# Optimization experiments

Measured on AMD Instinct MI355X. Metric: run time of the kernel, lower is better.

The kernel has to match this reference:

```python
import jax, jax.numpy as jnp
import numpy as np

B, T, C = 8, 2048, 1024
CONTEXT_SIZE = T  # repo ties context_size to sequence length of the mask


def setup_inputs() -> dict:
    key = jax.random.key(0)
    ks = jax.random.split(key, 7)
    s = 1.0 / np.sqrt(C)
    return {
        "x": jax.random.normal(ks[0], (B, T, C), dtype=jnp.float32),
        "Wq": jax.random.normal(ks[1], (C, C), dtype=jnp.float32) * s,
        "bq": jax.random.normal(ks[2], (C,), dtype=jnp.float32) * s,
        "Wk": jax.random.normal(ks[3], (C, C), dtype=jnp.float32) * s,
        "bk": jax.random.normal(ks[4], (C,), dtype=jnp.float32) * s,
        "Wv": jax.random.normal(ks[5], (C, C), dtype=jnp.float32) * s,
        "bv": jax.random.normal(ks[6], (C,), dtype=jnp.float32) * s,
    }


def reference(x, Wq, bq, Wk, bk, Wv, bv):
    # x: [B, T, C]; weights stored as [in, out] so y = x @ W + b (same math as nn.Linear)
    Tlen = x.shape[1]
    q = x @ Wq + bq
    k = x @ Wk + bk
    v = x @ Wv + bv
    # NOTE: original scales by context_size**-0.5 (seq-length based), not head-dim
    scale = jnp.asarray(CONTEXT_SIZE, x.dtype) ** -0.5
    scores = jnp.einsum("btc,bsc->bts", q, k) * scale  # [B, T, T]
    causal = jnp.tril(jnp.ones((Tlen, Tlen), dtype=bool))
    scores = jnp.where(causal, scores, -jnp.inf)
    attn = jax.nn.softmax(scores, axis=-1)
    return jnp.einsum("bts,bsc->btc", attn, v)
```

## Files before the change

### kernel.cpp

```cpp
#include <hip/hip_runtime.h>

#define B_SZ 8
#define T_SZ 2048
#define C_SZ 1024

typedef __attribute__((ext_vector_type(8))) short short8;
typedef __attribute__((ext_vector_type(8))) unsigned short ushort8;
typedef __attribute__((ext_vector_type(4))) float f32x4;

__device__ __forceinline__ unsigned short f2bf(float x) {
  union { float f; unsigned u; } v; v.f = x;
  unsigned r = v.u + 0x7FFFu + ((v.u >> 16) & 1u);
  return (unsigned short)(r >> 16);
}
__device__ __forceinline__ float bf2f(unsigned short h) {
  union { unsigned u; float f; } v; v.u = ((unsigned)h) << 16;
  return v.f;
}

__device__ __forceinline__ void gload16(const void* g, void* l) {
  __builtin_amdgcn_global_load_lds(
      (const __attribute__((address_space(1))) unsigned int*)(uintptr_t)g,
      (__attribute__((address_space(3))) unsigned int*)(uintptr_t)l, 16, 0, 0);
}

__device__ __forceinline__ int xcd_swz(int orig, int nwg) {
  return (orig & 7) * (nwg >> 3) + (orig >> 3);
}

#define WAITV(N) asm volatile("s_waitcnt vmcnt(" #N ")" ::: "memory")
#define BAR1                            \
  {                                     \
    asm volatile("" ::: "memory");      \
    __builtin_amdgcn_s_barrier();       \
    __builtin_amdgcn_sched_barrier(0);  \
    asm volatile("" ::: "memory");      \
  }
#define BAR2                            \
  {                                     \
    asm volatile("" ::: "memory");      \
    __builtin_amdgcn_s_barrier();       \
    asm volatile("" ::: "memory");      \
  }

template <int LDA, int LDB>
__device__ __forceinline__ void nt8p(const unsigned short* __restrict__ Ab,
                                     const unsigned short* __restrict__ Bb,
                                     const int NT, unsigned short* lds,
                                     f32x4 (&acc)[2][4][4]) {
  const int lane = threadIdx.x & 63;
  const int wid = threadIdx.x >> 6;
  const int wr = wid >> 2;
  const int wc = wid & 3;
  const int fr = lane & 15;
  const int fq = lane >> 4;

  const int aslot = ((lane & 7) ^ (lane >> 3)) * 8;
  const int rr0 = (wid * 2 + 0) * 8 + (lane >> 3);
  const int rr1 = (wid * 2 + 1) * 8 + (lane >> 3);
  const unsigned short* pA0 =
      Ab + (size_t)((rr0 >> 6) * 128 + (rr0 & 63)) * LDA + aslot;
  const unsigned short* pA1 =
      Ab + (size_t)((rr1 >> 6) * 128 + (rr1 & 63)) * LDA + aslot;
  const int bslot = ((lane & 3) ^ ((lane >> 3) & 3)) * 8;
  const unsigned short* pB0 =
      Bb + (size_t)((wid * 2 + 0) * 16 + (lane >> 2)) * LDB + bslot;
  const unsigned short* pB1 =
      Bb + (size_t)((wid * 2 + 1) * 16 + (lane >> 2)) * LDB + bslot;
  const int ldsC0 = (wid * 2 + 0) * 512;
  const int ldsC1 = (wid * 2 + 1) * 512;

  const int arb = wr * 4096 + fr * 64;
  const int asw0 = ((0 * 4 + fq) ^ (fr & 7)) * 8;
  const int asw1 = ((1 * 4 + fq) ^ (fr & 7)) * 8;
  const int brb =
      16384 + (wc * 64 + fr) * 32 + ((fq ^ ((fr >> 1) & 3)) * 8);

#define STG_A(d, h, kt)                                           \
  {                                                               \
    gload16(pA0 + (size_t)(h) * 64 * LDA + (size_t)(kt) * 64,     \
            lds + (d) * 32768 + (h) * 8192 + ldsC0);              \
    gload16(pA1 + (size_t)(h) * 64 * LDA + (size_t)(kt) * 64,     \
            lds + (d) * 32768 + (h) * 8192 + ldsC1);              \
  }
#define STG_B(d, kh, kt)                                          \
  {                                                               \
    gload16(pB0 + (kh) * 32 + (size_t)(kt) * 64,                  \
            lds + (d) * 32768 + 16384 + (kh) * 8192 + ldsC0);     \
    gload16(pB1 + (kh) * 32 + (size_t)(kt) * 64,                  \
            lds + (d) * 32768 + 16384 + (kh) * 8192 + ldsC1);     \
  }
#define LDAF(d, r, s)                                             \
  _Pragma("unroll") for (int mb = 0; mb < 4; ++mb) af[mb] =       \
      *(const short8*)&lds[(d) * 32768 + (r) * 8192 + arb +       \
                           mb * 1024 + ((s) ? asw1 : asw0)];
#define LDBF(d, s)                                                \
  _Pragma("unroll") for (int nb = 0; nb < 4; ++nb) bf[nb] =       \
      *(const short8*)&lds[(d) * 32768 + (s) * 8192 + brb + nb * 512];
#define MM(r)                                                     \
  __builtin_amdgcn_s_setprio(1);                                  \
  _Pragma("unroll") for (int mb = 0; mb < 4; ++mb)                \
  _Pragma("unroll") for (int nb = 0; nb < 4; ++nb)                \
  acc[r][mb][nb] = __builtin_amdgcn_mfma_f32_16x16x32_bf16(       \
      af[mb], bf[nb], acc[r][mb][nb], 0, 0, 0);                   \
  __builtin_amdgcn_s_setprio(0);
#define TILE_STEP(d, dn, TT)                                                 \
  {                                                                          \
    const int tp1 = ((TT) + 1 < NT) ? (TT) + 1 : NT - 1;                     \
    const int tp2 = ((TT) + 2 < NT) ? (TT) + 2 : NT - 1;                     \
    short8 af[4], bf[4];                                                     \
    LDAF(d, 0, 0); LDBF(d, 0); STG_B(dn, 1, tp1); BAR1; MM(0); WAITV(6); BAR2; \
    LDAF(d, 1, 0); STG_A(dn, 1, tp1); BAR1; MM(1); BAR2;                     \
    LDAF(d, 0, 1); LDBF(d, 1); STG_B(d, 0, tp2); BAR1; MM(0); BAR2;          \
    LDAF(d, 1, 1); STG_A(d, 0, tp2); BAR1; MM(1); WAITV(8); BAR2;            \
  }

  const int t1 = (NT > 1) ? 1 : 0;
  STG_B(0, 0, 0);
  STG_A(0, 0, 0);
  STG_B(0, 1, 0);
  STG_A(0, 1, 0);
  STG_B(1, 0, t1);
  STG_A(1, 0, t1);
  WAITV(8);
  BAR2;

  for (int T = 0; T < NT; T += 2) {
    TILE_STEP(0, 1, T);
    TILE_STEP(1, 0, T + 1);
  }
#undef STG_A
#undef STG_B
#undef LDAF
#undef LDBF
#undef MM
#undef TILE_STEP
}

__global__ __launch_bounds__(256) void convert_x(const float* __restrict__ x,
                                                 unsigned short* __restrict__ Xb,
                                                 int n8) {
  for (int i = blockIdx.x * blockDim.x + threadIdx.x; i < n8;
       i += gridDim.x * blockDim.x) {
    const float4* p = (const float4*)(x + (size_t)i * 8);
    float4 a = p[0], b = p[1];
    ushort8 u;
    u[0] = f2bf(a.x); u[1] = f2bf(a.y); u[2] = f2bf(a.z); u[3] = f2bf(a.w);
    u[4] = f2bf(b.x); u[5] = f2bf(b.y); u[6] = f2bf(b.z); u[7] = f2bf(b.w);
    *(ushort8*)(Xb + (size_t)i * 8) = u;
  }
}

__global__ __launch_bounds__(256) void transpose_w(
    const float* __restrict__ Wq, const float* __restrict__ Wk,
    const float* __restrict__ Wv, unsigned short* __restrict__ Wt) {
  const int z = blockIdx.z;
  const float* W = z == 0 ? Wq : (z == 1 ? Wk : Wv);
  unsigned short* O = Wt + (size_t)z * C_SZ * C_SZ;
  __shared__ float tl[32][33];
  const int bx = blockIdx.x * 32;
  const int by = blockIdx.y * 32;
  const int tx = threadIdx.x & 31;
  const int ty = threadIdx.x >> 5;
#pragma unroll
  for (int j = 0; j < 4; ++j)
    tl[ty + j * 8][tx] = W[(size_t)(by + ty + j * 8) * C_SZ + bx + tx];
  __syncthreads();
#pragma unroll
  for (int j = 0; j < 4; ++j)
    O[(size_t)(bx + ty + j * 8) * C_SZ + by + tx] = f2bf(tl[tx][ty + j * 8]);
}

__global__ __launch_bounds__(256) void transpose_v(
    const unsigned short* __restrict__ V, unsigned short* __restrict__ Vt) {
  const int b = blockIdx.z;
  __shared__ unsigned short tl[64][66];
  const int bx = blockIdx.x * 64;
  const int by = blockIdx.y * 64;
  const int tx = threadIdx.x & 63;
  const int ty = threadIdx.x >> 6;
  const unsigned short* Vb = V + (size_t)b * T_SZ * C_SZ;
  unsigned short* Ob = Vt + (size_t)b * C_SZ * T_SZ;
#pragma unroll
  for (int r = 0; r < 16; ++r)
    tl[ty * 16 + r][tx] = Vb[(size_t)(by + ty * 16 + r) * C_SZ + bx + tx];
  __syncthreads();
#pragma unroll
  for (int r = 0; r < 16; ++r)
    Ob[(size_t)(bx + ty * 16 + r) * T_SZ + by + tx] = tl[tx][ty * 16 + r];
}

__global__ __launch_bounds__(512, 1) void qkv_fused(
    const unsigned short* __restrict__ Xb, const unsigned short* __restrict__ Wt,
    const float* __restrict__ bq, const float* __restrict__ bk,
    const float* __restrict__ bv, unsigned short* __restrict__ QKV) {
  __shared__ unsigned short lds[65536] __attribute__((aligned(128)));
  const int wg = xcd_swz(blockIdx.x, 3 * 64 * 4);
  const int z = wg >> 8;
  const int rem = wg & 255;
  const int m0 = (rem >> 2) * 256;
  const int n0 = (rem & 3) * 256;
  const float* bias = z == 0 ? bq : (z == 1 ? bk : bv);

  f32x4 acc[2][4][4] = {};
  nt8p<C_SZ, C_SZ>(Xb + (size_t)m0 * C_SZ,
                   Wt + (size_t)z * C_SZ * C_SZ + (size_t)n0 * C_SZ,
                   C_SZ / 64, lds, acc);

  unsigned short* Y = QKV + (size_t)z * B_SZ * T_SZ * C_SZ;
  const int lane = threadIdx.x & 63;
  const int wid = threadIdx.x >> 6;
  const int wr = wid >> 2, wc = wid & 3;
  const int fr = lane & 15, fq = lane >> 4;
#pragma unroll
  for (int r = 0; r < 2; ++r)
#pragma unroll
    for (int nb = 0; nb < 4; ++nb) {
      const int col = n0 + wc * 64 + nb * 16 + fr;
      const float bvv = bias[col];
#pragma unroll
      for (int mb = 0; mb < 4; ++mb) {
        const int row0 = m0 + wr * 128 + r * 64 + mb * 16 + fq * 4;
#pragma unroll
        for (int j = 0; j < 4; ++j)
          Y[(size_t)(row0 + j) * C_SZ + col] = f2bf(acc[r][mb][nb][j] + bvv);
      }
    }
}

__global__ __launch_bounds__(512, 1) void scores_gemm(
    const unsigned short* __restrict__ Q, const unsigned short* __restrict__ Km,
    unsigned short* __restrict__ S, float scale) {
  const int wg = xcd_swz(blockIdx.x, B_SZ * 8 * 8);
  const int b = wg >> 6;
  const int rem = wg & 63;
  const int mt = rem >> 3, nt = rem & 7;
  if (nt > mt) return;
  const int m0 = mt * 256, n0 = nt * 256;
  __shared__ unsigned short lds[65536] __attribute__((aligned(128)));

  f32x4 acc[2][4][4] = {};
  nt8p<C_SZ, C_SZ>(Q + (size_t)b * T_SZ * C_SZ + (size_t)m0 * C_SZ,
                   Km + (size_t)b * T_SZ * C_SZ + (size_t)n0 * C_SZ,
                   C_SZ / 64, lds, acc);

  unsigned short* Sb = S + (size_t)b * T_SZ * T_SZ;
  const int lane = threadIdx.x & 63;
  const int wid = threadIdx.x >> 6;
  const int wr = wid >> 2, wc = wid & 3;
  const int fr = lane & 15, fq = lane >> 4;
#pragma unroll
  for (int r = 0; r < 2; ++r)
#pragma unroll
    for (int nb = 0; nb < 4; ++nb) {
      const int col = n0 + wc * 64 + nb * 16 + fr;
#pragma unroll
      for (int mb = 0; mb < 4; ++mb) {
        const int row0 = m0 + wr * 128 + r * 64 + mb * 16 + fq * 4;
#pragma unroll
        for (int j = 0; j < 4; ++j)
          Sb[(size_t)(row0 + j) * T_SZ + col] = f2bf(acc[r][mb][nb][j] * scale);
      }
    }
}

__device__ __forceinline__ float wredmax(float v) {
#pragma unroll
  for (int o = 32; o > 0; o >>= 1) v = fmaxf(v, __shfl_xor(v, o, 64));
  return v;
}
__device__ __forceinline__ float wredsum(float v) {
#pragma unroll
  for (int o = 32; o > 0; o >>= 1) v += __shfl_xor(v, o, 64);
  return v;
}

__global__ __launch_bounds__(256) void softmax_causal(
    unsigned short* __restrict__ S) {
  const int row = blockIdx.x;
  const int b = row >> 11;
  const int tq = row & (T_SZ - 1);
  unsigned short* sr = S + (size_t)b * T_SZ * T_SZ + (size_t)tq * T_SZ;
  const int len = tq + 1;
  const int wlen = (len + 255) & ~255;
  const int tid = threadIdx.x;
  const int lane = tid & 63;
  const int wid = tid >> 6;
  const int i0 = tid * 8;
  __shared__ float red[4];

  const ushort8 raw = *(const ushort8*)(sr + i0);
  float v[8];
  float mx = -1e30f;
#pragma unroll
  for (int j = 0; j < 8; ++j) {
    v[j] = (i0 + j < len) ? bf2f(raw[j]) : -1e30f;
    mx = fmaxf(mx, v[j]);
  }
  mx = wredmax(mx);
  if (lane == 0) red[wid] = mx;
  __syncthreads();
  mx = fmaxf(fmaxf(red[0], red[1]), fmaxf(red[2], red[3]));
  __syncthreads();

  float sm = 0.f;
#pragma unroll
  for (int j = 0; j < 8; ++j) {
    v[j] = __expf(v[j] - mx);
    sm += v[j];
  }
  sm = wredsum(sm);
  if (lane == 0) red[wid] = sm;
  __syncthreads();
  sm = red[0] + red[1] + red[2] + red[3];
  const float inv = 1.f / sm;

  if (i0 < wlen) {
    ushort8 o;
#pragma unroll
    for (int j = 0; j < 8; ++j)
      o[j] = (i0 + j < len) ? f2bf(v[j] * inv) : (unsigned short)0;
    *(ushort8*)(sr + i0) = o;
  }
}

__global__ __launch_bounds__(512, 1) void pv_gemm(
    const unsigned short* __restrict__ P, const unsigned short* __restrict__ Vt,
    float* __restrict__ O) {
  const int wg = xcd_swz(blockIdx.x, B_SZ * 8 * 4);
  const int b = wg >> 5;
  const int rem = wg & 31;
  const int mt = rem >> 2, nt = rem & 3;
  const int m0 = mt * 256, n0 = nt * 256;
  __shared__ unsigned short lds[65536] __attribute__((aligned(128)));

  f32x4 acc[2][4][4] = {};
  nt8p<T_SZ, T_SZ>(P + (size_t)b * T_SZ * T_SZ + (size_t)m0 * T_SZ,
                   Vt + (size_t)b * C_SZ * T_SZ + (size_t)n0 * T_SZ,
                   4 * (mt + 1), lds, acc);

  float* Ob = O + (size_t)b * T_SZ * C_SZ;
  const int lane = threadIdx.x & 63;
  const int wid = threadIdx.x >> 6;
  const int wr = wid >> 2, wc = wid & 3;
  const int fr = lane & 15, fq = lane >> 4;
#pragma unroll
  for (int r = 0; r < 2; ++r)
#pragma unroll
    for (int nb = 0; nb < 4; ++nb) {
      const int col = n0 + wc * 64 + nb * 16 + fr;
#pragma unroll
      for (int mb = 0; mb < 4; ++mb) {
        const int row0 = m0 + wr * 128 + r * 64 + mb * 16 + fq * 4;
#pragma unroll
        for (int j = 0; j < 4; ++j)
          Ob[(size_t)(row0 + j) * C_SZ + col] = acc[r][mb][nb][j];
      }
    }
}

extern "C" void kernel_launch(void* const* d_in, const int* in_sizes, int n_in,
                              void* d_out, int out_size, void* d_ws,
                              size_t ws_size, hipStream_t stream) {
  (void)in_sizes; (void)n_in; (void)out_size; (void)ws_size;
  const float* x = (const float*)d_in[0];
  const float* Wq = (const float*)d_in[1];
  const float* bq = (const float*)d_in[2];
  const float* Wk = (const float*)d_in[3];
  const float* bk = (const float*)d_in[4];
  const float* Wv = (const float*)d_in[5];
  const float* bv = (const float*)d_in[6];
  float* out = (float*)d_out;

  const size_t TC = (size_t)B_SZ * T_SZ * C_SZ;
  unsigned short* Q = (unsigned short*)d_ws;
  unsigned short* K = Q + TC;
  unsigned short* V = K + TC;
  unsigned short* S = V + TC;
  unsigned short* Xb = S;
  unsigned short* Wt = S + TC;
  unsigned short* Vt = Q;

  const float scale = 0.022097086912079608f;

  hipLaunchKernelGGL(convert_x, dim3(2048), dim3(256), 0, stream, x, Xb,
                     (int)(TC / 8));
  hipLaunchKernelGGL(transpose_w, dim3(32, 32, 3), dim3(256), 0, stream, Wq,
                     Wk, Wv, Wt);
  hipLaunchKernelGGL(qkv_fused, dim3(3 * 64 * 4), dim3(512), 0, stream, Xb, Wt,
                     bq, bk, bv, Q);
  hipLaunchKernelGGL(scores_gemm, dim3(B_SZ * 8 * 8), dim3(512), 0, stream, Q,
                     K, S, scale);
  hipLaunchKernelGGL(transpose_v, dim3(16, 32, 8), dim3(256), 0, stream, V,
                     Vt);
  hipLaunchKernelGGL(softmax_causal, dim3(B_SZ * T_SZ), dim3(256), 0, stream,
                     S);
  hipLaunchKernelGGL(pv_gemm, dim3(B_SZ * 8 * 4), dim3(512), 0, stream, S, Vt,
                     out);
}
```

Baseline: 268.8 us.

## Double-buffer LDS fragment reads across MFMA phases, raise occupancy, skip masked softmax loads

Restructures the GEMM main loop so A/B fragments for the next phase are read from LDS into a second register set while the current MFMA batch runs, hiding LDS latency. Launch bounds for the three GEMM kernels change from 1 to 2 blocks per SM, which caps registers per thread. That cap may cause spills given the larger live fragment set, and the 128KB LDS per block likely still allows only one block. Softmax also skips loading the fully masked tail of each causal row.

```diff
diff --git a/kernel.cpp b/kernel.cpp
--- a/kernel.cpp
+++ b/kernel.cpp
@@ -73,8 +73,9 @@
   const int arb = wr * 4096 + fr * 64;
   const int asw0 = ((0 * 4 + fq) ^ (fr & 7)) * 8;
   const int asw1 = ((1 * 4 + fq) ^ (fr & 7)) * 8;
-  const int brb =
-      16384 + (wc * 64 + fr) * 32 + ((fq ^ ((fr >> 1) & 3)) * 8);
+  const int brb = 16384 + (wc * 64 + fr) * 32 + ((fq ^ ((fr >> 1) & 3)) * 8);
+
+  short8 afq[4], afp[4], bf0[4], bf1[4];
 
 #define STG_A(d, h, kt)                                           \
   {                                                               \
@@ -90,40 +91,57 @@
     gload16(pB1 + (kh) * 32 + (size_t)(kt) * 64,                  \
             lds + (d) * 32768 + 16384 + (kh) * 8192 + ldsC1);     \
   }
-#define LDAF(d, r, s)                                             \
-  _Pragma("unroll") for (int mb = 0; mb < 4; ++mb) af[mb] =       \
-      *(const short8*)&lds[(d) * 32768 + (r) * 8192 + arb +       \
+#define RD_A(dst, d, h, s)                                        \
+  _Pragma("unroll") for (int mb = 0; mb < 4; ++mb) dst[mb] =      \
+      *(const short8*)&lds[(d) * 32768 + (h) * 8192 + arb +       \
                            mb * 1024 + ((s) ? asw1 : asw0)];
-#define LDBF(d, s)                                                \
-  _Pragma("unroll") for (int nb = 0; nb < 4; ++nb) bf[nb] =       \
+#define RD_B(dst, d, s)                                           \
+  _Pragma("unroll") for (int nb = 0; nb < 4; ++nb) dst[nb] =      \
       *(const short8*)&lds[(d) * 32768 + (s) * 8192 + brb + nb * 512];
-#define MM(r)                                                     \
+#define MMQ(r, AF, BF)                                            \
   __builtin_amdgcn_s_setprio(1);                                  \
   _Pragma("unroll") for (int mb = 0; mb < 4; ++mb)                \
   _Pragma("unroll") for (int nb = 0; nb < 4; ++nb)                \
   acc[r][mb][nb] = __builtin_amdgcn_mfma_f32_16x16x32_bf16(       \
-      af[mb], bf[nb], acc[r][mb][nb], 0, 0, 0);                   \
+      AF[mb], BF[nb], acc[r][mb][nb], 0, 0, 0);                   \
   __builtin_amdgcn_s_setprio(0);
-#define TILE_STEP(d, dn, TT)                                                 \
-  {                                                                          \
-    const int tp1 = ((TT) + 1 < NT) ? (TT) + 1 : NT - 1;                     \
-    const int tp2 = ((TT) + 2 < NT) ? (TT) + 2 : NT - 1;                     \
-    short8 af[4], bf[4];                                                     \
-    LDAF(d, 0, 0); LDBF(d, 0); STG_B(dn, 1, tp1); BAR1; MM(0); WAITV(6); BAR2; \
-    LDAF(d, 1, 0); STG_A(dn, 1, tp1); BAR1; MM(1); BAR2;                     \
-    LDAF(d, 0, 1); LDBF(d, 1); STG_B(d, 0, tp2); BAR1; MM(0); BAR2;          \
-    LDAF(d, 1, 1); STG_A(d, 0, tp2); BAR1; MM(1); WAITV(8); BAR2;            \
+
+#define TILE_STEP(d, dn, TT)                                                  \
+  {                                                                           \
+    const int tp1 = ((TT) + 1 < NT) ? (TT) + 1 : NT - 1;                      \
+    const int tp2 = ((TT) + 2 < NT) ? (TT) + 2 : NT - 1;                      \
+                                                                      \
+    RD_A(afp, d, 1, 0);                                                       \
+    STG_B(dn, 1, tp1);                                                        \
+    BAR1; MMQ(0, afq, bf0); BAR2;                                             \
+                                                                      \
+    WAITV(8);                                                                 \
+    RD_A(afq, d, 0, 1); RD_B(bf1, d, 1);                                      \
+    STG_A(dn, 1, tp1);                                                        \
+    BAR1; MMQ(1, afp, bf0); BAR2;                                             \
+                                                                      \
+    WAITV(8);                                                                 \
+    RD_A(afp, d, 1, 1);                                                       \
+    STG_B(d, 0, tp2);                                                         \
+    BAR1; MMQ(0, afq, bf1); BAR2;                                             \
+                                                                      \
+    WAITV(6);                                                                 \
+    RD_A(afq, dn, 0, 0); RD_B(bf0, dn, 0);                                    \
+    STG_A(d, 0, tp2);                                                         \
+    BAR1; MMQ(1, afp, bf1); BAR2;                                             \
   }
 
   const int t1 = (NT > 1) ? 1 : 0;
+  STG_A(0, 0, 0);
   STG_B(0, 0, 0);
-  STG_A(0, 0, 0);
   STG_B(0, 1, 0);
   STG_A(0, 1, 0);
   STG_B(1, 0, t1);
   STG_A(1, 0, t1);
   WAITV(8);
   BAR2;
+  RD_A(afq, 0, 0, 0);
+  RD_B(bf0, 0, 0);
 
   for (int T = 0; T < NT; T += 2) {
     TILE_STEP(0, 1, T);
@@ -131,9 +149,9 @@
   }
 #undef STG_A
 #undef STG_B
-#undef LDAF
-#undef LDBF
-#undef MM
+#undef RD_A
+#undef RD_B
+#undef MMQ
 #undef TILE_STEP
 }
 
@@ -190,7 +208,7 @@
     Ob[(size_t)(bx + ty * 16 + r) * T_SZ + by + tx] = tl[tx][ty * 16 + r];
 }
 
-__global__ __launch_bounds__(512, 1) void qkv_fused(
+__global__ __launch_bounds__(512, 2) void qkv_fused(
     const unsigned short* __restrict__ Xb, const unsigned short* __restrict__ Wt,
     const float* __restrict__ bq, const float* __restrict__ bk,
     const float* __restrict__ bv, unsigned short* __restrict__ QKV) {
@@ -228,7 +246,7 @@
     }
 }
 
-__global__ __launch_bounds__(512, 1) void scores_gemm(
+__global__ __launch_bounds__(512, 2) void scores_gemm(
     const unsigned short* __restrict__ Q, const unsigned short* __restrict__ Km,
     unsigned short* __restrict__ S, float scale) {
   const int wg = xcd_swz(blockIdx.x, B_SZ * 8 * 8);
@@ -289,13 +307,18 @@
   const int i0 = tid * 8;
   __shared__ float red[4];
 
-  const ushort8 raw = *(const ushort8*)(sr + i0);
   float v[8];
   float mx = -1e30f;
-#pragma unroll
-  for (int j = 0; j < 8; ++j) {
-    v[j] = (i0 + j < len) ? bf2f(raw[j]) : -1e30f;
-    mx = fmaxf(mx, v[j]);
+  if (i0 < len) {
+    const ushort8 raw = *(const ushort8*)(sr + i0);
+#pragma unroll
+    for (int j = 0; j < 8; ++j) {
+      v[j] = (i0 + j < len) ? bf2f(raw[j]) : -1e30f;
+      mx = fmaxf(mx, v[j]);
+    }
+  } else {
+#pragma unroll
+    for (int j = 0; j < 8; ++j) v[j] = -1e30f;
   }
   mx = wredmax(mx);
   if (lane == 0) red[wid] = mx;
@@ -324,7 +347,7 @@
   }
 }
 
-__global__ __launch_bounds__(512, 1) void pv_gemm(
+__global__ __launch_bounds__(512, 2) void pv_gemm(
     const unsigned short* __restrict__ P, const unsigned short* __restrict__ Vt,
     float* __restrict__ O) {
   const int wg = xcd_swz(blockIdx.x, B_SZ * 8 * 4);
```

After: 268.8 us. Within noise of the previous version (-0.0%).
